# Kernel tuning notes

Measured on AMD Instinct MI355X. Metric: run time of the kernel, lower is better.

## Reference

```python
import jax, jax.numpy as jnp
import numpy as np

B, T, C, H = 4, 2048, 1024, 1024

def setup_inputs() -> dict:
    key = jax.random.key(0)
    ks = jax.random.split(key, 7)
    s = 0.02
    return {
        "x": jax.random.normal(ks[0], (B, T, C), dtype=jnp.float32),
        "k": jax.random.normal(ks[1], (B, T, C), dtype=jnp.float32),
        "q": jax.random.normal(ks[2], (B, T, C), dtype=jnp.float32),
        "v": jax.random.normal(ks[3], (B, T, C), dtype=jnp.float32),
        "Wk": jax.random.normal(ks[4], (C, H), dtype=jnp.float32) * s,
        "Wq": jax.random.normal(ks[5], (C, H), dtype=jnp.float32) * s,
        "Wv": jax.random.normal(ks[6], (C, H), dtype=jnp.float32) * s,
    }

def reference(x, k, q, v, Wk, Wq, Wv):
    Tcur = x.shape[1]
    kp = jnp.einsum('btc,ch->bth', k, Wk)
    qp = jnp.einsum('btc,ch->bth', q, Wq)
    # NOTE: original torch code (faithfully) projects v with the QUERY weights
    vp = jnp.einsum('btc,ch->bth', v, Wq)
    scale = jnp.asarray(H, jnp.float32) ** -0.5
    weights = jnp.einsum('bth,bsh->bts', qp, kp) * scale  # [B,T,T]
    causal = jnp.tril(jnp.ones((Tcur, Tcur), dtype=bool))
    weights = jnp.where(causal, weights, -jnp.inf)
    weights = jax.nn.softmax(weights, axis=-1)
    # dropout p=0.0 -> identity
    out = jnp.einsum('bts,bsh->bth', weights, vp)
    return out
```

## Files before the change

kernel.cpp:

```cpp
#include <hip/hip_runtime.h>
#include <stdint.h>

typedef unsigned short u16;
typedef __attribute__((ext_vector_type(8))) short short8;
typedef __attribute__((ext_vector_type(8))) u16 ushort8;
typedef __attribute__((ext_vector_type(4))) float floatx4;

__device__ __forceinline__ u16 f2bf(float f) {
  union { float f; unsigned u; } c; c.f = f;
  unsigned u = c.u;
  return (u16)((u + 0x7fffu + ((u >> 16) & 1u)) >> 16);
}
__device__ __forceinline__ float bf2f(u16 h) {
  union { unsigned u; float f; } c; c.u = (unsigned)h << 16;
  return c.f;
}

__device__ __forceinline__ void async16(const u16* g, u16* l) {
  auto* gp = reinterpret_cast<const __attribute__((address_space(1))) uint32_t*>(
      reinterpret_cast<uintptr_t>(g));
  auto* lp = reinterpret_cast<__attribute__((address_space(3))) uint32_t*>(
      reinterpret_cast<uintptr_t>(l));
  __builtin_amdgcn_global_load_lds(gp, lp, 16, 0, 0);
}

template <int BN, int OUT_BF16>
__global__ __launch_bounds__(512) void gemm_bt(
    const u16* __restrict__ A, const u16* __restrict__ B, void* __restrict__ Cv,
    int K, int lda, int ldb, int ldc,
    long long sA, long long sB, long long sC,
    float scale, int causal_skip, int causal_klimit) {
  const int m0 = blockIdx.x * 128;
  const int n0 = blockIdx.y * BN;
  if (causal_skip && n0 >= m0 + 128) return;
  A += (size_t)blockIdx.z * sA;
  B += (size_t)blockIdx.z * sB;

  __shared__ u16 As[128 * 32];
  __shared__ u16 Bs[BN * 32];

  const int tid = threadIdx.x;
  const int lane = tid & 63;
  const int wid = tid >> 6;
  constexpr int WN = BN / 4;
  constexpr int FN = WN / 16;
  const int wm = (wid & 1) * 64;
  const int wn = (wid >> 1) * WN;
  const int fr = lane & 15;
  const int fq = lane >> 4;

  floatx4 acc[4][FN] = {};

  int kt_end = K >> 5;
  if (causal_klimit) {
    int lim = (m0 >> 5) + 4;
    if (lim < kt_end) kt_end = lim;
  }

  const int rowi = tid >> 2;
  const int segi = tid & 3;
  const u16* gA = A + (size_t)(m0 + rowi) * lda + segi * 8;
  const u16* gB = B + (size_t)(n0 + rowi) * ldb + segi * 8;
  u16* lA = &As[tid * 8];
  u16* lB = &Bs[tid * 8];

  for (int kt = 0; kt < kt_end; ++kt) {
    const int k0 = kt << 5;
    async16(gA + k0, lA);
    async16(gB + k0, lB);
    if (BN == 256) async16(gB + k0 + (size_t)128 * ldb, lB + 4096);
    __builtin_amdgcn_s_waitcnt(0);
    __syncthreads();

    short8 av[4], bv[FN];
#pragma unroll
    for (int i = 0; i < 4; ++i)
      av[i] = *(const short8*)&As[(wm + i * 16 + fr) * 32 + fq * 8];
#pragma unroll
    for (int j = 0; j < FN; ++j)
      bv[j] = *(const short8*)&Bs[(wn + j * 16 + fr) * 32 + fq * 8];

#pragma unroll
    for (int i = 0; i < 4; ++i)
#pragma unroll
      for (int j = 0; j < FN; ++j)
        acc[i][j] = __builtin_amdgcn_mfma_f32_16x16x32_bf16(av[i], bv[j],
                                                            acc[i][j], 0, 0, 0);
    __syncthreads();
  }

  if (OUT_BF16) {
    u16* C = (u16*)Cv + (size_t)blockIdx.z * sC;
#pragma unroll
    for (int i = 0; i < 4; ++i) {
      const int m = m0 + wm + i * 16 + fq * 4;
#pragma unroll
      for (int j = 0; j < FN; ++j) {
        const int n = n0 + wn + j * 16 + fr;
#pragma unroll
        for (int r = 0; r < 4; ++r)
          C[(size_t)(m + r) * ldc + n] = f2bf(acc[i][j][r] * scale);
      }
    }
  } else {
    float* C = (float*)Cv + (size_t)blockIdx.z * sC;
#pragma unroll
    for (int i = 0; i < 4; ++i) {
      const int m = m0 + wm + i * 16 + fq * 4;
#pragma unroll
      for (int j = 0; j < FN; ++j) {
        const int n = n0 + wn + j * 16 + fr;
#pragma unroll
        for (int r = 0; r < 4; ++r)
          C[(size_t)(m + r) * ldc + n] = acc[i][j][r] * scale;
      }
    }
  }
}

__global__ __launch_bounds__(256) void cast3(
    const float* __restrict__ q, const float* __restrict__ k,
    const float* __restrict__ v, u16* __restrict__ out, int n8) {
  int i = blockIdx.x * 256 + threadIdx.x;
  if (i >= n8) return;
  const float* src = blockIdx.y == 0 ? q : (blockIdx.y == 1 ? k : v);
  u16* dst = out + (size_t)blockIdx.y * n8 * 8;
  floatx4 a = ((const floatx4*)src)[i * 2];
  floatx4 b = ((const floatx4*)src)[i * 2 + 1];
  ushort8 o;
#pragma unroll
  for (int j = 0; j < 4; ++j) { o[j] = f2bf(a[j]); o[4 + j] = f2bf(b[j]); }
  ((ushort8*)dst)[i] = o;
}

__global__ __launch_bounds__(256) void transpose_cast64(
    const float* __restrict__ in, u16* __restrict__ out, int R, int C) {
  __shared__ u16 tile[64][72];
  const int r0 = blockIdx.x * 64;
  const int c0 = blockIdx.y * 64;
  const int tid = threadIdx.x;
#pragma unroll
  for (int rnd = 0; rnd < 2; ++rnd) {
    int e = rnd * 256 + tid;
    int rr = e >> 3, seg = e & 7;
    const float* p = &in[(size_t)(r0 + rr) * C + c0 + seg * 8];
    floatx4 a = *(const floatx4*)p;
    floatx4 b = *(const floatx4*)(p + 4);
    u16* tp = &tile[rr][seg * 8];
#pragma unroll
    for (int j = 0; j < 4; ++j) { tp[j] = f2bf(a[j]); tp[4 + j] = f2bf(b[j]); }
  }
  __syncthreads();
#pragma unroll
  for (int rnd = 0; rnd < 2; ++rnd) {
    int e = rnd * 256 + tid;
    int cc = e >> 3, rseg = e & 7;
    ushort8 tv;
#pragma unroll
    for (int j = 0; j < 8; ++j) tv[j] = tile[rseg * 8 + j][cc];
    *(ushort8*)&out[(size_t)(c0 + cc) * R + r0 + rseg * 8] = tv;
  }
}

__global__ __launch_bounds__(256) void transpose64(
    const u16* __restrict__ in, u16* __restrict__ out, int R, int C) {
  __shared__ u16 tile[64][72];
  const size_t boff = (size_t)blockIdx.z * R * C;
  const int r0 = blockIdx.x * 64;
  const int c0 = blockIdx.y * 64;
  const int tid = threadIdx.x;
#pragma unroll
  for (int rnd = 0; rnd < 2; ++rnd) {
    int e = rnd * 256 + tid;
    int rr = e >> 3, seg = e & 7;
    ushort8 v = *(const ushort8*)&in[boff + (size_t)(r0 + rr) * C + c0 + seg * 8];
    *(ushort8*)&tile[rr][seg * 8] = v;
  }
  __syncthreads();
#pragma unroll
  for (int rnd = 0; rnd < 2; ++rnd) {
    int e = rnd * 256 + tid;
    int cc = e >> 3, rseg = e & 7;
    ushort8 tv;
#pragma unroll
    for (int j = 0; j < 8; ++j) tv[j] = tile[rseg * 8 + j][cc];
    *(ushort8*)&out[boff + (size_t)(c0 + cc) * R + r0 + rseg * 8] = tv;
  }
}

__global__ __launch_bounds__(256) void softmax_causal(u16* __restrict__ S,
                                                      int T) {
  const int row = blockIdx.x;
  const int t = row & (T - 1);
  const int len = t + 1;
  u16* srow = S + (size_t)row * T;
  const int tid = threadIdx.x;

  float vals[8];
  int cnt = 0;
  float mx = -1e30f;
  for (int i = tid; i < len; i += 256) {
    float v = bf2f(srow[i]);
    vals[cnt++] = v;
    mx = fmaxf(mx, v);
  }
  __shared__ float red[4];
#pragma unroll
  for (int o = 32; o > 0; o >>= 1) mx = fmaxf(mx, __shfl_down(mx, o, 64));
  if ((tid & 63) == 0) red[tid >> 6] = mx;
  __syncthreads();
  mx = fmaxf(fmaxf(red[0], red[1]), fmaxf(red[2], red[3]));
  __syncthreads();

  float sum = 0.f;
  for (int c = 0; c < cnt; ++c) {
    vals[c] = __expf(vals[c] - mx);
    sum += vals[c];
  }
#pragma unroll
  for (int o = 32; o > 0; o >>= 1) sum += __shfl_down(sum, o, 64);
  if ((tid & 63) == 0) red[tid >> 6] = sum;
  __syncthreads();
  sum = red[0] + red[1] + red[2] + red[3];
  const float inv = 1.f / sum;

  int c = 0;
  for (int i = tid; i < len; i += 256) srow[i] = f2bf(vals[c++] * inv);
  for (int i = tid; i < T; i += 256)
    if (i >= len) srow[i] = 0;
}

extern "C" void kernel_launch(void* const* d_in, const int* in_sizes, int n_in,
                              void* d_out, int out_size, void* d_ws,
                              size_t ws_size, hipStream_t stream) {
  (void)in_sizes; (void)n_in; (void)out_size; (void)ws_size;
  const float* k  = (const float*)d_in[1];
  const float* q  = (const float*)d_in[2];
  const float* v  = (const float*)d_in[3];
  const float* Wk = (const float*)d_in[4];
  const float* Wq = (const float*)d_in[5];
  float* out = (float*)d_out;

  const int B = 4, T = 2048, C = 1024, H = 1024;
  const int M = B * T;
  const size_t MC = (size_t)M * C, CH = (size_t)C * H, MH = (size_t)M * H;

  u16* qkv  = (u16*)d_ws;
  u16* WT   = qkv + 3 * MC;
  u16* qkvp = WT + 3 * CH;
  u16* Sb   = qkvp + 3 * MH;
  u16* vpT  = qkv;

  const int n8 = (int)(MC / 8);
  cast3<<<dim3(n8 / 256, 3), 256, 0, stream>>>(q, k, v, qkv, n8);
  transpose_cast64<<<dim3(C / 64, H / 64), 256, 0, stream>>>(Wq, WT, C, H);
  transpose_cast64<<<dim3(C / 64, H / 64), 256, 0, stream>>>(Wk, WT + CH, C, H);
  transpose_cast64<<<dim3(C / 64, H / 64), 256, 0, stream>>>(Wq, WT + 2 * CH, C, H);

  gemm_bt<256, 1><<<dim3(M / 128, H / 256, 3), 512, 0, stream>>>(
      qkv, WT, qkvp, C, C, C, H,
      (long long)MC, (long long)CH, (long long)MH, 1.f, 0, 0);

  transpose64<<<dim3(T / 64, H / 64, B), 256, 0, stream>>>(
      qkvp + 2 * MH, vpT, T, H);

  gemm_bt<128, 1><<<dim3(T / 128, T / 128, B), 512, 0, stream>>>(
      qkvp, qkvp + MH, Sb, H, H, H, T,
      (long long)T * H, (long long)T * H, (long long)T * T, 0.03125f, 1, 0);

  softmax_causal<<<dim3(B * T), 256, 0, stream>>>(Sb, T);

  gemm_bt<128, 0><<<dim3(T / 128, H / 128, B), 512, 0, stream>>>(
      Sb, vpT, out, T, T, T, H,
      (long long)T * T, (long long)H * T, (long long)T * H, 1.f, 0, 1);
}
```

Baseline: 362.5 us.

## Fuse V transpose into projection GEMM, swizzle LDS, retile to 256 threads

The projection GEMM now writes the V projection straight into a transposed layout from its epilogue, which removes the separate transpose kernel. The three weight transpose-casts are merged into one launch. The GEMM uses 256 threads with a 128x128 tile and 4x4 MFMA fragments per wave, and applies an XOR swizzle to LDS rows to cut bank conflicts on fragment reads. The transposed V store writes only 4 contiguous bf16 values per thread, so that store may be poorly coalesced, and each thread now holds more accumulators, which raises register pressure.

```diff
diff --git a/kernel.cpp b/kernel.cpp
--- a/kernel.cpp
+++ b/kernel.cpp
@@ -4,6 +4,7 @@
 typedef unsigned short u16;
 typedef __attribute__((ext_vector_type(8))) short short8;
 typedef __attribute__((ext_vector_type(8))) u16 ushort8;
+typedef __attribute__((ext_vector_type(4))) u16 u16x4;
 typedef __attribute__((ext_vector_type(4))) float floatx4;
 
 __device__ __forceinline__ u16 f2bf(float f) {
@@ -24,32 +25,31 @@
   __builtin_amdgcn_global_load_lds(gp, lp, 16, 0, 0);
 }
 
-template <int BN, int OUT_BF16>
-__global__ __launch_bounds__(512) void gemm_bt(
+template <int OUT_BF16>
+__global__ __launch_bounds__(256) void gemm_bt(
     const u16* __restrict__ A, const u16* __restrict__ B, void* __restrict__ Cv,
     int K, int lda, int ldb, int ldc,
     long long sA, long long sB, long long sC,
-    float scale, int causal_skip, int causal_klimit) {
+    float scale, int causal_skip, int causal_klimit,
+    int vpt, u16* __restrict__ vpC) {
   const int m0 = blockIdx.x * 128;
-  const int n0 = blockIdx.y * BN;
+  const int n0 = blockIdx.y * 128;
   if (causal_skip && n0 >= m0 + 128) return;
   A += (size_t)blockIdx.z * sA;
   B += (size_t)blockIdx.z * sB;
 
   __shared__ u16 As[128 * 32];
-  __shared__ u16 Bs[BN * 32];
+  __shared__ u16 Bs[128 * 32];
 
   const int tid = threadIdx.x;
   const int lane = tid & 63;
   const int wid = tid >> 6;
-  constexpr int WN = BN / 4;
-  constexpr int FN = WN / 16;
   const int wm = (wid & 1) * 64;
-  const int wn = (wid >> 1) * WN;
+  const int wn = (wid >> 1) * 64;
   const int fr = lane & 15;
   const int fq = lane >> 4;
 
-  floatx4 acc[4][FN] = {};
+  floatx4 acc[4][4] = {};
 
   int kt_end = K >> 5;
   if (causal_klimit) {
@@ -59,43 +59,69 @@
 
   const int rowi = tid >> 2;
   const int segi = tid & 3;
-  const u16* gA = A + (size_t)(m0 + rowi) * lda + segi * 8;
-  const u16* gB = B + (size_t)(n0 + rowi) * ldb + segi * 8;
+  const int sgz = segi ^ ((rowi >> 1) & 3);
+  const u16* gA = A + (size_t)(m0 + rowi) * lda + sgz * 8;
+  const u16* gB = B + (size_t)(n0 + rowi) * ldb + sgz * 8;
   u16* lA = &As[tid * 8];
   u16* lB = &Bs[tid * 8];
+
+  const u16* rdA[4];
+  const u16* rdB[4];
+#pragma unroll
+  for (int i = 0; i < 4; ++i) {
+    int ra = wm + i * 16 + fr;
+    rdA[i] = &As[ra * 32 + (fq ^ ((ra >> 1) & 3)) * 8];
+    int rb = wn + i * 16 + fr;
+    rdB[i] = &Bs[rb * 32 + (fq ^ ((rb >> 1) & 3)) * 8];
+  }
 
   for (int kt = 0; kt < kt_end; ++kt) {
     const int k0 = kt << 5;
     async16(gA + k0, lA);
+    async16(gA + k0 + (size_t)64 * lda, lA + 2048);
     async16(gB + k0, lB);
-    if (BN == 256) async16(gB + k0 + (size_t)128 * ldb, lB + 4096);
+    async16(gB + k0 + (size_t)64 * ldb, lB + 2048);
     __builtin_amdgcn_s_waitcnt(0);
     __syncthreads();
 
-    short8 av[4], bv[FN];
+    short8 av[4], bv[4];
+#pragma unroll
+    for (int i = 0; i < 4; ++i) av[i] = *(const short8*)rdA[i];
+#pragma unroll
+    for (int j = 0; j < 4; ++j) bv[j] = *(const short8*)rdB[j];
+
 #pragma unroll
     for (int i = 0; i < 4; ++i)
-      av[i] = *(const short8*)&As[(wm + i * 16 + fr) * 32 + fq * 8];
-#pragma unroll
-    for (int j = 0; j < FN; ++j)
-      bv[j] = *(const short8*)&Bs[(wn + j * 16 + fr) * 32 + fq * 8];
-
-#pragma unroll
-    for (int i = 0; i < 4; ++i)
-#pragma unroll
-      for (int j = 0; j < FN; ++j)
+#pragma unroll
+      for (int j = 0; j < 4; ++j)
         acc[i][j] = __builtin_amdgcn_mfma_f32_16x16x32_bf16(av[i], bv[j],
                                                             acc[i][j], 0, 0, 0);
     __syncthreads();
   }
 
+  if (vpt && blockIdx.z == 2) {
+#pragma unroll
+    for (int i = 0; i < 4; ++i) {
+      const int m = m0 + wm + i * 16 + fq * 4;
+      const int b = m >> 11, t = m & 2047;
+#pragma unroll
+      for (int j = 0; j < 4; ++j) {
+        const int n = n0 + wn + j * 16 + fr;
+        u16x4 o;
+#pragma unroll
+        for (int r = 0; r < 4; ++r) o[r] = f2bf(acc[i][j][r]);
+        *(u16x4*)&vpC[(size_t)b * 2097152 + (size_t)n * 2048 + t] = o;
+      }
+    }
+    return;
+  }
   if (OUT_BF16) {
     u16* C = (u16*)Cv + (size_t)blockIdx.z * sC;
 #pragma unroll
     for (int i = 0; i < 4; ++i) {
       const int m = m0 + wm + i * 16 + fq * 4;
 #pragma unroll
-      for (int j = 0; j < FN; ++j) {
+      for (int j = 0; j < 4; ++j) {
         const int n = n0 + wn + j * 16 + fr;
 #pragma unroll
         for (int r = 0; r < 4; ++r)
@@ -108,7 +134,7 @@
     for (int i = 0; i < 4; ++i) {
       const int m = m0 + wm + i * 16 + fq * 4;
 #pragma unroll
-      for (int j = 0; j < FN; ++j) {
+      for (int j = 0; j < 4; ++j) {
         const int n = n0 + wn + j * 16 + fr;
 #pragma unroll
         for (int r = 0; r < 4; ++r)
@@ -133,9 +159,12 @@
   ((ushort8*)dst)[i] = o;
 }
 
-__global__ __launch_bounds__(256) void transpose_cast64(
-    const float* __restrict__ in, u16* __restrict__ out, int R, int C) {
+__global__ __launch_bounds__(256) void transpose_castW(
+    const float* __restrict__ Wq, const float* __restrict__ Wk,
+    u16* __restrict__ out, int R, int C) {
   __shared__ u16 tile[64][72];
+  const float* in = (blockIdx.z == 1) ? Wk : Wq;
+  u16* dst = out + (size_t)blockIdx.z * R * C;
   const int r0 = blockIdx.x * 64;
   const int c0 = blockIdx.y * 64;
   const int tid = threadIdx.x;
@@ -158,33 +187,7 @@
     ushort8 tv;
 #pragma unroll
     for (int j = 0; j < 8; ++j) tv[j] = tile[rseg * 8 + j][cc];
-    *(ushort8*)&out[(size_t)(c0 + cc) * R + r0 + rseg * 8] = tv;
-  }
-}
-
-__global__ __launch_bounds__(256) void transpose64(
-    const u16* __restrict__ in, u16* __restrict__ out, int R, int C) {
-  __shared__ u16 tile[64][72];
-  const size_t boff = (size_t)blockIdx.z * R * C;
-  const int r0 = blockIdx.x * 64;
-  const int c0 = blockIdx.y * 64;
-  const int tid = threadIdx.x;
-#pragma unroll
-  for (int rnd = 0; rnd < 2; ++rnd) {
-    int e = rnd * 256 + tid;
-    int rr = e >> 3, seg = e & 7;
-    ushort8 v = *(const ushort8*)&in[boff + (size_t)(r0 + rr) * C + c0 + seg * 8];
-    *(ushort8*)&tile[rr][seg * 8] = v;
-  }
-  __syncthreads();
-#pragma unroll
-  for (int rnd = 0; rnd < 2; ++rnd) {
-    int e = rnd * 256 + tid;
-    int cc = e >> 3, rseg = e & 7;
-    ushort8 tv;
-#pragma unroll
-    for (int j = 0; j < 8; ++j) tv[j] = tile[rseg * 8 + j][cc];
-    *(ushort8*)&out[boff + (size_t)(c0 + cc) * R + r0 + rseg * 8] = tv;
+    *(ushort8*)&dst[(size_t)(c0 + cc) * R + r0 + rseg * 8] = tv;
   }
 }
 
@@ -248,29 +251,26 @@
   u16* qkv  = (u16*)d_ws;
   u16* WT   = qkv + 3 * MC;
   u16* qkvp = WT + 3 * CH;
-  u16* Sb   = qkvp + 3 * MH;
-  u16* vpT  = qkv;
+  u16* vpT  = qkvp + 2 * MH;
+  u16* Sb   = vpT + MH;
 
   const int n8 = (int)(MC / 8);
   cast3<<<dim3(n8 / 256, 3), 256, 0, stream>>>(q, k, v, qkv, n8);
-  transpose_cast64<<<dim3(C / 64, H / 64), 256, 0, stream>>>(Wq, WT, C, H);
-  transpose_cast64<<<dim3(C / 64, H / 64), 256, 0, stream>>>(Wk, WT + CH, C, H);
-  transpose_cast64<<<dim3(C / 64, H / 64), 256, 0, stream>>>(Wq, WT + 2 * CH, C, H);
-
-  gemm_bt<256, 1><<<dim3(M / 128, H / 256, 3), 512, 0, stream>>>(
+  transpose_castW<<<dim3(C / 64, H / 64, 3), 256, 0, stream>>>(Wq, Wk, WT, C, H);
+
+  gemm_bt<1><<<dim3(M / 128, H / 128, 3), 256, 0, stream>>>(
       qkv, WT, qkvp, C, C, C, H,
-      (long long)MC, (long long)CH, (long long)MH, 1.f, 0, 0);
-
-  transpose64<<<dim3(T / 64, H / 64, B), 256, 0, stream>>>(
-      qkvp + 2 * MH, vpT, T, H);
-
-  gemm_bt<128, 1><<<dim3(T / 128, T / 128, B), 512, 0, stream>>>(
+      (long long)MC, (long long)CH, (long long)MH, 1.f, 0, 0, 1, vpT);
+
+  gemm_bt<1><<<dim3(T / 128, T / 128, B), 256, 0, stream>>>(
       qkvp, qkvp + MH, Sb, H, H, H, T,
-      (long long)T * H, (long long)T * H, (long long)T * T, 0.03125f, 1, 0);
+      (long long)T * H, (long long)T * H, (long long)T * T,
+      0.03125f, 1, 0, 0, nullptr);
 
   softmax_causal<<<dim3(B * T), 256, 0, stream>>>(Sb, T);
 
-  gemm_bt<128, 0><<<dim3(T / 128, H / 128, B), 512, 0, stream>>>(
+  gemm_bt<0><<<dim3(T / 128, H / 128, B), 256, 0, stream>>>(
       Sb, vpT, out, T, T, T, H,
-      (long long)T * T, (long long)H * T, (long long)T * H, 1.f, 0, 1);
-}
+      (long long)T * T, (long long)H * T, (long long)T * H,
+      1.f, 0, 1, 0, nullptr);
+}
```

Measured after the change: 359.6 us. No clear change (-0.8%).
